# Optimization experiments

Measured on AMD Instinct MI355X. Metric: run time of the kernel, lower is better.

The kernel has to match this reference:

```python
import jax, jax.numpy as jnp
import numpy as np

T_STEP = 0.01
N_STEPS = 1000
H_S = 64
N_TARGETS = 2048
INPUT_S = 2
H_NN = 256
ACTION_S = 2


def setup_inputs() -> dict:
    key = jax.random.key(0)
    ks = jax.random.split(key, 9)
    target = jax.random.normal(ks[0], (N_TARGETS, INPUT_S), dtype=jnp.float32)
    D = jax.random.normal(ks[1], (H_S,), dtype=jnp.float32) * 0.1
    P = jax.random.normal(ks[2], (H_S, H_S), dtype=jnp.float32)
    l1_w = jax.random.normal(ks[3], (H_NN, INPUT_S), dtype=jnp.float32) * 0.05
    l1_b = jax.random.normal(ks[4], (H_NN,), dtype=jnp.float32) * 0.05
    l2_w = jax.random.normal(ks[5], (H_S, H_NN), dtype=jnp.float32) * 0.05
    l2_b = jax.random.normal(ks[6], (H_S,), dtype=jnp.float32) * 0.05
    lm_w = jax.random.normal(ks[7], (ACTION_S, H_S), dtype=jnp.float32) * 0.05
    lm_b = jax.random.normal(ks[8], (ACTION_S,), dtype=jnp.float32) * 0.05
    return {"target": target, "D": D, "P": P,
            "l1_w": l1_w, "l1_b": l1_b, "l2_w": l2_w, "l2_b": l2_b,
            "lm_w": lm_w, "lm_b": lm_b}


def reference(target, D, P, l1_w, l1_b, l2_w, l2_b, lm_w, lm_b):
    # initial condition MLP: relu(l1) -> l2, then transpose to (h_s, n_targets)
    h = jax.nn.relu(target @ l1_w.T + l1_b)           # (n_targets, h_nn)
    x0 = (h @ l2_w.T + l2_b).T                        # (h_s, n_targets)
    # A = P diag(exp(D)) P^-1 ; step map x <- (I - dt*A) x
    A = (P * jnp.exp(D)[None, :]) @ jnp.linalg.inv(P)  # (h_s, h_s)
    M = jnp.eye(H_S, dtype=A.dtype) - T_STEP * A

    def step(x, _):
        act = jnp.tanh(x.T @ lm_w.T + lm_b)            # (n_targets, action_s)
        return M @ x, (x, act)

    _, (hidden_states, acts) = jax.lax.scan(step, x0, None, length=N_STEPS)
    # hidden_states: (n_steps, h_s, n_targets); acts: (n_steps, n_targets, action_s)
    actions = jnp.transpose(acts, (1, 2, 0))           # (n_targets, action_s, n_steps)
    return actions, hidden_states
```

## Files before the change

### kernel.cpp

```cpp
#include <hip/hip_runtime.h>
#include <math.h>

#define NT 2048
#define HS 64
#define HNN 256
#define NSTEPS 1000
#define TSTEP 0.01f

typedef unsigned short u16;
typedef __attribute__((ext_vector_type(8))) short bf16x8;
typedef __attribute__((ext_vector_type(4))) float f32x4;

#define OFF_HT   148736

#define S_H 1028

__device__ inline void bsplit(float x, u16& hi, u16& lo) {
    unsigned u = __float_as_uint(x);
    unsigned r = (u + 0x7FFFu + ((u >> 16) & 1u)) >> 16;
    hi = (u16)r;
    float xh = __uint_as_float(r << 16);
    float d = x - xh;
    unsigned v = __float_as_uint(d);
    unsigned s = (v + 0x7FFFu + ((v >> 16) & 1u)) >> 16;
    lo = (u16)s;
}

__device__ inline void bar_lds() {
    asm volatile("s_waitcnt lgkmcnt(0)" ::: "memory");
    __builtin_amdgcn_s_barrier();
    asm volatile("" ::: "memory");
}

__device__ inline float tanh_fast(float x) {
    float xc = fminf(fmaxf(x, -15.f), 15.f);
    float a = __builtin_amdgcn_exp2f(xc * 2.885390082f);
    return (a - 1.f) * __builtin_amdgcn_rcpf(a + 1.f);
}

struct FrontSh {
    float Aug[64 * 73];
    float shT[256 * 9];
    float y0s[64 * 9];
    float fvec[2][64];
    float tgt[8][2];
    float lam_s[64], l2l_s[64];
    float Q_s[128];
    float us[8 * 128];
};

__global__ __launch_bounds__(512) void k_front(const float* __restrict__ target,
                                               const float* __restrict__ l1_w,
                                               const float* __restrict__ l1_b,
                                               const float* __restrict__ l2_w,
                                               const float* __restrict__ l2_b,
                                               const float* __restrict__ lm_w,
                                               const float* __restrict__ lm_b,
                                               const float* __restrict__ D,
                                               const float* __restrict__ P,
                                               float* __restrict__ ws,
                                               float* __restrict__ actions) {
    __shared__ FrontSh sh;
    int ct = blockIdx.x;
    int cbase = ct * 8;
    int tid = threadIdx.x;

    for (int idx = tid; idx < 4096; idx += 512) {
        int r = idx >> 6, c = idx & 63;
        sh.Aug[r * 73 + c] = P[r * 64 + c];
    }
    if (tid >= 448 && tid < 456) {
        int c = tid - 448;
        float2 tv = ((const float2*)target)[cbase + c];
        sh.tgt[c][0] = tv.x; sh.tgt[c][1] = tv.y;
    } else if (tid >= 256 && tid < 320) {
        int i = tid - 256;
        float l = 1.0f - TSTEP * expf(D[i]);
        sh.lam_s[i] = l;
        sh.l2l_s[i] = log2f(l);
    } else if (tid >= 320 && tid < 448) {
        int t = tid - 320;
        int a = t >> 6, i = t & 63;
        float s = 0.f;
        for (int r = 0; r < 64; ++r) s = fmaf(lm_w[a * 64 + r], P[r * 64 + i], s);
        sh.Q_s[t] = s;
    }
    __syncthreads();

    if (tid < 256) {
        float w0 = l1_w[2 * tid], w1 = l1_w[2 * tid + 1], bb = l1_b[tid];
        #pragma unroll
        for (int cc = 0; cc < 8; ++cc)
            sh.shT[tid * 9 + cc] =
                fmaxf(fmaf(w0, sh.tgt[cc][0], fmaf(w1, sh.tgt[cc][1], bb)), 0.f);
    }
    __syncthreads();

    int i = tid >> 3, c = tid & 7;
    {
        const float* l2wi = l2_w + i * 256;
        float a0 = l2_b[i], a1 = 0, a2 = 0, a3 = 0;
        #pragma unroll 4
        for (int j = 0; j < 256; j += 4) {
            a0 = fmaf(l2wi[j],     sh.shT[j * 9 + c],       a0);
            a1 = fmaf(l2wi[j + 1], sh.shT[(j + 1) * 9 + c], a1);
            a2 = fmaf(l2wi[j + 2], sh.shT[(j + 2) * 9 + c], a2);
            a3 = fmaf(l2wi[j + 3], sh.shT[(j + 3) * 9 + c], a3);
        }
        sh.Aug[i * 73 + 64 + c] = (a0 + a1) + (a2 + a3);
    }
    if (tid < 64) {
        float nv = sh.Aug[tid * 73];
        float pv = __shfl(nv, 0);
        sh.fvec[0][tid] = (tid == 0) ? 0.f : nv * __builtin_amdgcn_rcpf(pv);
    }
    __syncthreads();

    for (int t = 0; t < 64; ++t) {
        int par = t & 1;
        if (tid < 64) {
            int col0 = (t < 63) ? (t + 1) : 64;
            float f = sh.fvec[par][tid];
            float src = sh.Aug[t * 73 + col0];
            float nv = sh.Aug[tid * 73 + col0] - f * src;
            sh.Aug[tid * 73 + col0] = nv;
            if (t < 63) {
                float pv = __shfl(nv, t + 1);
                sh.fvec[par ^ 1][tid] = (tid == (t + 1)) ? 0.f
                                        : nv * __builtin_amdgcn_rcpf(pv);
            }
        } else {
            int w = (tid >> 6) - 1;
            int lane = tid & 63;
            float f = sh.fvec[par][lane];
            const float* rowp = sh.Aug + t * 73;
            float* rowr = sh.Aug + lane * 73;
            int pcnt = 62 - t;
            int smax = pcnt + 8;
            for (int s = 1 + w; s <= smax; s += 7) {
                int col = (s <= pcnt) ? (t + 1 + s) : (64 + (s - pcnt - 1));
                rowr[col] -= f * rowp[col];
            }
        }
        __syncthreads();
    }

    sh.y0s[i * 9 + c] = sh.Aug[i * 73 + 64 + c]
                        * __builtin_amdgcn_rcpf(sh.Aug[i * 73 + i]);
    __syncthreads();

    for (int idx = tid; idx < 1024; idx += 512) {
        int cgi = idx >> 7, t = idx & 127;
        sh.us[cgi * 128 + t] = sh.Q_s[t] * sh.y0s[(t & 63) * 9 + cgi];
    }
    if (tid < 128) {
        int kt = tid >> 6, lane = tid & 63;
        int c15 = lane & 15;
        if ((c15 >> 3) == (ct & 1)) {
            int cl = c15 & 7;
            int i0 = kt * 32 + (lane >> 4) * 8;
            u16* YH = (u16*)(ws + OFF_HT);
            u16* YL = YH + 131072;
            bf16x8 vh, vl;
            #pragma unroll
            for (int j = 0; j < 8; ++j) {
                u16 h, lo;
                bsplit(sh.y0s[(i0 + j) * 9 + cl], h, lo);
                vh[j] = (short)h; vl[j] = (short)lo;
            }
            int off = (((ct >> 1) * 2 + kt) * 64 + lane);
            *(bf16x8*)(YH + off * 8) = vh;
            *(bf16x8*)(YL + off * 8) = vl;
        }
    }
    __syncthreads();

    if (tid < 500) {
        int k0 = tid * 2;
        float b0 = lm_b[0], b1 = lm_b[1];
        float fk0 = (float)k0;
        float2 s[8][2];
        #pragma unroll
        for (int j = 0; j < 8; ++j) {
            s[j][0] = make_float2(b0, b0);
            s[j][1] = make_float2(b1, b1);
        }
        #pragma unroll 2
        for (int ii = 0; ii < 64; ++ii) {
            float p0 = __builtin_amdgcn_exp2f(fk0 * sh.l2l_s[ii]);
            float p1 = p0 * sh.lam_s[ii];
            #pragma unroll
            for (int j = 0; j < 8; ++j) {
                float u0 = sh.us[j * 128 + ii];
                float u1 = sh.us[j * 128 + 64 + ii];
                s[j][0].x = fmaf(u0, p0, s[j][0].x);
                s[j][0].y = fmaf(u0, p1, s[j][0].y);
                s[j][1].x = fmaf(u1, p0, s[j][1].x);
                s[j][1].y = fmaf(u1, p1, s[j][1].y);
            }
        }
        #pragma unroll
        for (int j = 0; j < 8; ++j)
            #pragma unroll
            for (int a = 0; a < 2; ++a) {
                float2 r;
                r.x = tanh_fast(s[j][a].x);
                r.y = tanh_fast(s[j][a].y);
                *(float2*)(actions + (size_t)(cbase + j) * 2000 + a * 1000 + k0) = r;
            }
    }
}

__global__ __launch_bounds__(512, 2) void k_hidden(const float* __restrict__ P,
                                                   const float* __restrict__ D,
                                                   const float* __restrict__ ws,
                                                   float* __restrict__ hidden) {
    int k = blockIdx.x;
    int tid = threadIdx.x;
    int wid = tid >> 6, lane = tid & 63;
    int l15 = lane & 15, lg = lane >> 4;

    extern __shared__ float stage[];
    __shared__ float lp_s[64];

    const u16* YH = (const u16*)(ws + OFF_HT);
    const u16* YL = YH + 131072;

    if (tid < 64) {
        float l = 1.0f - TSTEP * expf(D[tid]);
        lp_s[tid] = exp2f((float)k * log2f(l));
    }
    __syncthreads();

    bf16x8 ah[4][2], al[4][2];
    #pragma unroll
    for (int rt = 0; rt < 4; ++rt) {
        int r = rt * 16 + l15;
        #pragma unroll
        for (int kt = 0; kt < 2; ++kt) {
            int i0 = kt * 32 + lg * 8;
            #pragma unroll
            for (int j = 0; j < 8; ++j) {
                float v = P[r * 64 + i0 + j] * lp_s[i0 + j];
                u16 h, lo;
                bsplit(v, h, lo);
                ah[rt][kt][j] = (short)h;
                al[rt][kt][j] = (short)lo;
            }
        }
    }

    float* outk = hidden + (size_t)k * 64 * NT;

    #pragma unroll 1
    for (int half = 0; half < 2; ++half) {
        bf16x8 bh[8][2], bl[8][2];
        #pragma unroll
        for (int q = 0; q < 8; ++q)
            #pragma unroll
            for (int kt = 0; kt < 2; ++kt) {
                int ct_g = half * 64 + wid * 8 + q;
                int off = ((ct_g * 2 + kt) * 64 + lane) * 8;
                bh[q][kt] = *(const bf16x8*)(YH + off);
                bl[q][kt] = *(const bf16x8*)(YL + off);
            }
        #pragma unroll
        for (int rt = 0; rt < 4; ++rt) {
            #pragma unroll
            for (int q = 0; q < 8; ++q) {
                f32x4 acc = {0.f, 0.f, 0.f, 0.f};
                #pragma unroll
                for (int kt = 0; kt < 2; ++kt) {
                    acc = __builtin_amdgcn_mfma_f32_16x16x32_bf16(ah[rt][kt], bh[q][kt], acc, 0, 0, 0);
                    acc = __builtin_amdgcn_mfma_f32_16x16x32_bf16(al[rt][kt], bh[q][kt], acc, 0, 0, 0);
                    acc = __builtin_amdgcn_mfma_f32_16x16x32_bf16(ah[rt][kt], bl[q][kt], acc, 0, 0, 0);
                }
                int col = wid * 128 + q * 16 + l15;
                #pragma unroll
                for (int reg = 0; reg < 4; ++reg)
                    stage[(lg * 4 + reg) * S_H + col] = acc[reg];
            }
            bar_lds();
            #pragma unroll
            for (int it = 0; it < 8; ++it) {
                int f = it * 512 + tid;
                int r = f >> 8, c4 = f & 255;
                float4 v = *(const float4*)&stage[r * S_H + (c4 << 2)];
                *(float4*)(outk + (size_t)(rt * 16 + r) * NT + half * 1024 + (c4 << 2)) = v;
            }
            bar_lds();
        }
    }
}

extern "C" void kernel_launch(void* const* d_in, const int* in_sizes, int n_in,
                              void* d_out, int out_size, void* d_ws, size_t ws_size,
                              hipStream_t stream) {
    const float* target = (const float*)d_in[0];
    const float* D      = (const float*)d_in[1];
    const float* P      = (const float*)d_in[2];
    const float* l1_w   = (const float*)d_in[3];
    const float* l1_b   = (const float*)d_in[4];
    const float* l2_w   = (const float*)d_in[5];
    const float* l2_b   = (const float*)d_in[6];
    const float* lm_w   = (const float*)d_in[7];
    const float* lm_b   = (const float*)d_in[8];
    float* ws = (float*)d_ws;
    float* actions = (float*)d_out;
    float* hidden  = (float*)d_out + 4096000;

    hipFuncSetAttribute((const void*)k_hidden,
                        hipFuncAttributeMaxDynamicSharedMemorySize, 16 * S_H * 4);

    hipLaunchKernelGGL(k_front,  dim3(256),  dim3(512), 0, stream,
                       target, l1_w, l1_b, l2_w, l2_b, lm_w, lm_b, D, P, ws, actions);
    hipLaunchKernelGGL(k_hidden, dim3(1000), dim3(512), 16 * S_H * 4, stream, P, D, ws, hidden);
}
```

Measured before the change: 165.5 us.

## Split hidden kernel per half and use per-wave LDS staging without barriers

```diff
diff --git a/kernel.cpp b/kernel.cpp
--- a/kernel.cpp
+++ b/kernel.cpp
@@ -13,7 +13,7 @@
 
 #define OFF_HT   148736
 
-#define S_H 1028
+#define SW 68
 
 __device__ inline void bsplit(float x, u16& hi, u16& lo) {
     unsigned u = __float_as_uint(x);
@@ -24,12 +24,6 @@
     unsigned v = __float_as_uint(d);
     unsigned s = (v + 0x7FFFu + ((v >> 16) & 1u)) >> 16;
     lo = (u16)s;
-}
-
-__device__ inline void bar_lds() {
-    asm volatile("s_waitcnt lgkmcnt(0)" ::: "memory");
-    __builtin_amdgcn_s_barrier();
-    asm volatile("" ::: "memory");
 }
 
 __device__ inline float tanh_fast(float x) {
@@ -215,12 +209,13 @@
                                                    const float* __restrict__ D,
                                                    const float* __restrict__ ws,
                                                    float* __restrict__ hidden) {
-    int k = blockIdx.x;
+    int bid = blockIdx.x;
+    int k = bid >> 1, half = bid & 1;
     int tid = threadIdx.x;
     int wid = tid >> 6, lane = tid & 63;
     int l15 = lane & 15, lg = lane >> 4;
 
-    extern __shared__ float stage[];
+    __shared__ float stage[8][16 * SW];
     __shared__ float lp_s[64];
 
     const u16* YH = (const u16*)(ws + OFF_HT);
@@ -249,46 +244,43 @@
             }
         }
     }
-
-    float* outk = hidden + (size_t)k * 64 * NT;
-
-    #pragma unroll 1
-    for (int half = 0; half < 2; ++half) {
-        bf16x8 bh[8][2], bl[8][2];
-        #pragma unroll
-        for (int q = 0; q < 8; ++q)
-            #pragma unroll
-            for (int kt = 0; kt < 2; ++kt) {
-                int ct_g = half * 64 + wid * 8 + q;
-                int off = ((ct_g * 2 + kt) * 64 + lane) * 8;
-                bh[q][kt] = *(const bf16x8*)(YH + off);
-                bl[q][kt] = *(const bf16x8*)(YL + off);
-            }
-        #pragma unroll
-        for (int rt = 0; rt < 4; ++rt) {
-            #pragma unroll
-            for (int q = 0; q < 8; ++q) {
+    bf16x8 bh[8][2], bl[8][2];
+    #pragma unroll
+    for (int t = 0; t < 8; ++t)
+        #pragma unroll
+        for (int kt = 0; kt < 2; ++kt) {
+            int ct_g = half * 64 + wid * 8 + t;
+            int off = ((ct_g * 2 + kt) * 64 + lane) * 8;
+            bh[t][kt] = *(const bf16x8*)(YH + off);
+            bl[t][kt] = *(const bf16x8*)(YL + off);
+        }
+
+    float* outw = hidden + (size_t)k * 64 * NT + half * 1024 + wid * 128;
+    float* st = stage[wid];
+
+    #pragma unroll
+    for (int rt = 0; rt < 4; ++rt) {
+        #pragma unroll
+        for (int qg = 0; qg < 2; ++qg) {
+            #pragma unroll
+            for (int q = 0; q < 4; ++q) {
                 f32x4 acc = {0.f, 0.f, 0.f, 0.f};
                 #pragma unroll
                 for (int kt = 0; kt < 2; ++kt) {
-                    acc = __builtin_amdgcn_mfma_f32_16x16x32_bf16(ah[rt][kt], bh[q][kt], acc, 0, 0, 0);
-                    acc = __builtin_amdgcn_mfma_f32_16x16x32_bf16(al[rt][kt], bh[q][kt], acc, 0, 0, 0);
-                    acc = __builtin_amdgcn_mfma_f32_16x16x32_bf16(ah[rt][kt], bl[q][kt], acc, 0, 0, 0);
+                    acc = __builtin_amdgcn_mfma_f32_16x16x32_bf16(ah[rt][kt], bh[qg * 4 + q][kt], acc, 0, 0, 0);
+                    acc = __builtin_amdgcn_mfma_f32_16x16x32_bf16(al[rt][kt], bh[qg * 4 + q][kt], acc, 0, 0, 0);
+                    acc = __builtin_amdgcn_mfma_f32_16x16x32_bf16(ah[rt][kt], bl[qg * 4 + q][kt], acc, 0, 0, 0);
                 }
-                int col = wid * 128 + q * 16 + l15;
                 #pragma unroll
                 for (int reg = 0; reg < 4; ++reg)
-                    stage[(lg * 4 + reg) * S_H + col] = acc[reg];
-            }
-            bar_lds();
-            #pragma unroll
-            for (int it = 0; it < 8; ++it) {
-                int f = it * 512 + tid;
-                int r = f >> 8, c4 = f & 255;
-                float4 v = *(const float4*)&stage[r * S_H + (c4 << 2)];
-                *(float4*)(outk + (size_t)(rt * 16 + r) * NT + half * 1024 + (c4 << 2)) = v;
-            }
-            bar_lds();
+                    st[(lg * 4 + reg) * SW + q * 16 + l15] = acc[reg];
+            }
+            #pragma unroll
+            for (int r4 = 0; r4 < 4; ++r4) {
+                int row = r4 * 4 + (lane >> 4);
+                f32x4 v = *(const f32x4*)&st[row * SW + (lane & 15) * 4];
+                *(f32x4*)(outw + (size_t)(rt * 16 + row) * NT + qg * 64 + (lane & 15) * 4) = v;
+            }
         }
     }
 }
@@ -309,10 +301,7 @@
     float* actions = (float*)d_out;
     float* hidden  = (float*)d_out + 4096000;
 
-    hipFuncSetAttribute((const void*)k_hidden,
-                        hipFuncAttributeMaxDynamicSharedMemorySize, 16 * S_H * 4);
-
     hipLaunchKernelGGL(k_front,  dim3(256),  dim3(512), 0, stream,
                        target, l1_w, l1_b, l2_w, l2_b, lm_w, lm_b, D, P, ws, actions);
-    hipLaunchKernelGGL(k_hidden, dim3(1000), dim3(512), 16 * S_H * 4, stream, P, D, ws, hidden);
-}
+    hipLaunchKernelGGL(k_hidden, dim3(2000), dim3(512), 0, stream, P, D, ws, hidden);
+}
```

Result: slower. 183.3 us (+10.7%).
